# Optimization experiments

Measured on AMD Instinct MI355X. Metric: run time of the kernel, lower is better.

The kernel has to match this reference:

```python
import jax, jax.numpy as jnp
import numpy as np

D_HEAD = 64
SCALE = 1.0 / (D_HEAD ** 0.5)
B, H, S = 4, 16, 2048

def setup_inputs() -> dict:
    key = jax.random.key(0)
    kq, kk, kv, km = jax.random.split(key, 4)
    query = jax.random.normal(kq, (B, H, S, D_HEAD), dtype=jnp.float32)
    key_t = jax.random.normal(kk, (B, H, S, D_HEAD), dtype=jnp.float32)
    value = jax.random.normal(kv, (B, H, S, D_HEAD), dtype=jnp.float32)
    masked = jax.random.bernoulli(km, 0.5, (B, H, S, S))
    return {"query": query, "key": key_t, "value": value, "masked": masked}

def reference(query, key, value, masked):
    # scores = (Q K^T) * (1/sqrt(d_head)), mask filled with -1e9, softmax over last dim
    scores = jnp.einsum('bhqd,bhkd->bhqk', query, key) * SCALE
    scores = jnp.where(masked, jnp.float32(-1e9), scores)
    attn = jax.nn.softmax(scores, axis=-1)
    return jnp.einsum('bhqk,bhkd->bhqd', attn, value)
```

## Files before the change

### kernel.cpp

```cpp
#include <hip/hip_runtime.h>

namespace {

constexpr int D  = 64;
constexpr int S  = 2048;
constexpr int BQ = 64;
constexpr int BK = 64;
constexpr int NT = S / BK;
constexpr float SCALE = 0.125f;
constexpr int PP = 72;

typedef short s16x8 __attribute__((ext_vector_type(8)));
typedef float f32x4 __attribute__((ext_vector_type(4)));

__device__ inline unsigned cvt_pk_bf16(float a, float b) {
  unsigned r;
  asm("v_cvt_pk_bf16_f32 %0, %1, %2" : "=v"(r) : "v"(a), "v"(b));
  return r;
}

__device__ inline unsigned short f2bf(float f) {
  union { float f; unsigned u; } v; v.f = f;
  unsigned u = v.u + (0x7fffu + ((v.u >> 16) & 1u));
  return (unsigned short)(u >> 16);
}

__global__ __launch_bounds__(256)
void cvt_kv(const float* __restrict__ Kg, const float* __restrict__ Vg,
            unsigned short* __restrict__ Kw, unsigned short* __restrict__ Vw)
{
  __shared__ unsigned short vt[64 * 72];
  const int tid = threadIdx.x;
  const int kt = blockIdx.x, bh = blockIdx.y;
  const int k0 = kt * BK;

  #pragma unroll
  for (int i = 0; i < 4; ++i) {
    const int e4 = i * 256 + tid;
    const int r  = e4 >> 4;
    const int db = (e4 & 15) * 4;
    const size_t rowK = (size_t)bh * S + k0 + r;

    const float4 kf = *(const float4*)(Kg + rowK * D + db);
    const float4 vf = *(const float4*)(Vg + rowK * D + db);

    uint2 kk;
    kk.x = cvt_pk_bf16(kf.x, kf.y);
    kk.y = cvt_pk_bf16(kf.z, kf.w);
    *(uint2*)&Kw[rowK * D + db] = kk;

    const unsigned v01 = cvt_pk_bf16(vf.x, vf.y);
    const unsigned v23 = cvt_pk_bf16(vf.z, vf.w);
    vt[(db + 0) * 72 + r] = (unsigned short)(v01);
    vt[(db + 1) * 72 + r] = (unsigned short)(v01 >> 16);
    vt[(db + 2) * 72 + r] = (unsigned short)(v23);
    vt[(db + 3) * 72 + r] = (unsigned short)(v23 >> 16);
  }
  __syncthreads();

  const int d  = tid >> 2;
  const int bq = (tid & 3) * 16;
  const uint4 a = *(const uint4*)&vt[d * 72 + bq];
  const uint4 b = *(const uint4*)&vt[d * 72 + bq + 8];
  unsigned short* vrow = Vw + ((size_t)bh * D + d) * S + k0 + bq;
  *(uint4*)(vrow)     = a;
  *(uint4*)(vrow + 8) = b;
}

__global__ __launch_bounds__(256, 4)
void attn_fwd(const float* __restrict__ Qg,
              const unsigned short* __restrict__ Kw,
              const unsigned short* __restrict__ Vw,
              const int* __restrict__ Mg,
              float* __restrict__ Og)
{
  __shared__ unsigned short k_lds[BK * 64];
  __shared__ unsigned short vt_lds[D * 64];
  __shared__ unsigned short p_lds[4 * 16 * PP];

  const int tid  = threadIdx.x;
  const int lane = tid & 63;
  const int w    = tid >> 6;
  const int g    = lane >> 4;
  const int lq   = lane & 15;

  const int q0 = blockIdx.x * BQ;
  const int bh = blockIdx.y;

  const float* Qb = Qg + (size_t)bh * S * D;
  float* Ob = Og + (size_t)bh * S * D;
  const unsigned short* Kb = Kw + (size_t)bh * S * D;
  const unsigned short* Vb = Vw + (size_t)bh * D * S;
  const int* Mq = Mg + (size_t)bh * S * S + (size_t)(q0 + w * 16 + lq) * S;

  const int sr  = tid >> 2;
  const int sb  = (tid & 3) * 2;
  const int swz = sr & 7;
  const unsigned short* Ksrc0 = Kb + (size_t)sr * D + sb * 8;
  const unsigned short* Vsrc0 = Vb + (size_t)sr * S + sb * 8;

  s16x8 qf[2];
  {
    const float* qr = Qb + (size_t)(q0 + w * 16 + lq) * D;
    #pragma unroll
    for (int ks = 0; ks < 2; ++ks) {
      float4 a = *(const float4*)(qr + ks * 32 + g * 8);
      float4 b = *(const float4*)(qr + ks * 32 + g * 8 + 4);
      s16x8 t;
      t[0] = (short)f2bf(a.x * SCALE); t[1] = (short)f2bf(a.y * SCALE);
      t[2] = (short)f2bf(a.z * SCALE); t[3] = (short)f2bf(a.w * SCALE);
      t[4] = (short)f2bf(b.x * SCALE); t[5] = (short)f2bf(b.y * SCALE);
      t[6] = (short)f2bf(b.z * SCALE); t[7] = (short)f2bf(b.w * SCALE);
      qf[ks] = t;
    }
  }

  f32x4 o[4];
  #pragma unroll
  for (int i = 0; i < 4; ++i) { o[i][0]=0.f; o[i][1]=0.f; o[i][2]=0.f; o[i][3]=0.f; }
  float m_run = -INFINITY, l_run = 0.f;

  unsigned short* p_w = p_lds + w * 16 * PP;
  const int swzr = lq & 7;

  uint4 ka = *(const uint4*)(Ksrc0);
  uint4 kb = *(const uint4*)(Ksrc0 + 8);
  uint4 va = *(const uint4*)(Vsrc0);
  uint4 vb = *(const uint4*)(Vsrc0 + 8);
  uint4 mw[4];
  #pragma unroll
  for (int t = 0; t < 4; ++t) mw[t] = *(const uint4*)(Mq + 16 * t + 4 * g);

  for (int kt = 0; kt < NT; ++kt) {
    *(uint4*)&k_lds [sr * 64 + ((sb    ) ^ swz) * 8] = ka;
    *(uint4*)&k_lds [sr * 64 + ((sb + 1) ^ swz) * 8] = kb;
    *(uint4*)&vt_lds[sr * 64 + ((sb    ) ^ swz) * 8] = va;
    *(uint4*)&vt_lds[sr * 64 + ((sb + 1) ^ swz) * 8] = vb;

    asm volatile("s_waitcnt lgkmcnt(0)" ::: "memory");
    __builtin_amdgcn_sched_barrier(0);
    __builtin_amdgcn_s_barrier();

    const int kn = (kt + 1 < NT) ? (kt + 1) * BK : kt * BK;
    uint4 kan = *(const uint4*)(Ksrc0 + (size_t)kn * 64);
    uint4 kbn = *(const uint4*)(Ksrc0 + (size_t)kn * 64 + 8);
    uint4 van = *(const uint4*)(Vsrc0 + kn);
    uint4 vbn = *(const uint4*)(Vsrc0 + kn + 8);
    uint4 mwn[4];
    #pragma unroll
    for (int t = 0; t < 4; ++t) mwn[t] = *(const uint4*)(Mq + kn + 16 * t + 4 * g);

    f32x4 st[4];
    #pragma unroll
    for (int t = 0; t < 4; ++t) {
      f32x4 c; c[0]=0.f; c[1]=0.f; c[2]=0.f; c[3]=0.f;
      #pragma unroll
      for (int ks = 0; ks < 2; ++ks) {
        s16x8 a = *(const s16x8*)&k_lds[(16 * t + lq) * 64 + (((ks << 2) + g) ^ swzr) * 8];
        c = __builtin_amdgcn_mfma_f32_16x16x32_bf16(a, qf[ks], c, 0, 0, 0);
      }
      st[t] = c;
    }

    float mx = -INFINITY;
    #pragma unroll
    for (int t = 0; t < 4; ++t) {
      if (mw[t].x) st[t][0] = -1e9f;
      if (mw[t].y) st[t][1] = -1e9f;
      if (mw[t].z) st[t][2] = -1e9f;
      if (mw[t].w) st[t][3] = -1e9f;
      mx = fmaxf(mx, fmaxf(fmaxf(st[t][0], st[t][1]), fmaxf(st[t][2], st[t][3])));
    }
    mx = fmaxf(mx, __shfl_xor(mx, 16));
    mx = fmaxf(mx, __shfl_xor(mx, 32));
    const float m_new = fmaxf(m_run, mx);
    const float alpha = __expf(m_run - m_new);
    float rs = 0.f;
    #pragma unroll
    for (int t = 0; t < 4; ++t) {
      #pragma unroll
      for (int r = 0; r < 4; ++r) {
        float p = __expf(st[t][r] - m_new);
        st[t][r] = p;
        rs += p;
      }
    }
    rs += __shfl_xor(rs, 16);
    rs += __shfl_xor(rs, 32);
    l_run = l_run * alpha + rs;
    m_run = m_new;

    const float al0 = __shfl(alpha, 4 * g + 0);
    const float al1 = __shfl(alpha, 4 * g + 1);
    const float al2 = __shfl(alpha, 4 * g + 2);
    const float al3 = __shfl(alpha, 4 * g + 3);
    #pragma unroll
    for (int dt = 0; dt < 4; ++dt) {
      o[dt][0] *= al0; o[dt][1] *= al1; o[dt][2] *= al2; o[dt][3] *= al3;
    }

    #pragma unroll
    for (int t = 0; t < 4; ++t) {
      uint2 pk;
      pk.x = cvt_pk_bf16(st[t][0], st[t][1]);
      pk.y = cvt_pk_bf16(st[t][2], st[t][3]);
      *(uint2*)&p_w[lq * PP + 16 * t + 4 * g] = pk;
    }
    asm volatile("s_waitcnt lgkmcnt(0)" ::: "memory");
    __builtin_amdgcn_sched_barrier(0);

    const s16x8 pa0 = *(const s16x8*)&p_w[lq * PP + 0  + g * 8];
    const s16x8 pa1 = *(const s16x8*)&p_w[lq * PP + 32 + g * 8];
    #pragma unroll
    for (int dt = 0; dt < 4; ++dt) {
      s16x8 vb0 = *(const s16x8*)&vt_lds[(16 * dt + lq) * 64 + ((g    ) ^ swzr) * 8];
      s16x8 vb1 = *(const s16x8*)&vt_lds[(16 * dt + lq) * 64 + ((4 + g) ^ swzr) * 8];
      o[dt] = __builtin_amdgcn_mfma_f32_16x16x32_bf16(pa0, vb0, o[dt], 0, 0, 0);
      o[dt] = __builtin_amdgcn_mfma_f32_16x16x32_bf16(pa1, vb1, o[dt], 0, 0, 0);
    }

    __builtin_amdgcn_s_barrier();

    ka = kan; kb = kbn; va = van; vb = vbn;
    #pragma unroll
    for (int t = 0; t < 4; ++t) mw[t] = mwn[t];
  }

  const float linv = 1.0f / l_run;
  const float li0 = __shfl(linv, 4 * g + 0);
  const float li1 = __shfl(linv, 4 * g + 1);
  const float li2 = __shfl(linv, 4 * g + 2);
  const float li3 = __shfl(linv, 4 * g + 3);
  #pragma unroll
  for (int dt = 0; dt < 4; ++dt) {
    const int d = 16 * dt + lq;
    Ob[(size_t)(q0 + w * 16 + 4 * g + 0) * D + d] = o[dt][0] * li0;
    Ob[(size_t)(q0 + w * 16 + 4 * g + 1) * D + d] = o[dt][1] * li1;
    Ob[(size_t)(q0 + w * 16 + 4 * g + 2) * D + d] = o[dt][2] * li2;
    Ob[(size_t)(q0 + w * 16 + 4 * g + 3) * D + d] = o[dt][3] * li3;
  }
}

}

extern "C" void kernel_launch(void* const* d_in, const int* in_sizes, int n_in,
                              void* d_out, int out_size, void* d_ws, size_t ws_size,
                              hipStream_t stream) {
  const float* Q = (const float*)d_in[0];
  const float* K = (const float*)d_in[1];
  const float* V = (const float*)d_in[2];
  const int*   M = (const int*)d_in[3];
  float* O = (float*)d_out;

  unsigned short* Kw = (unsigned short*)d_ws;
  unsigned short* Vw = Kw + (size_t)4 * 16 * S * D;

  dim3 cgrid(NT, 4 * 16);
  hipLaunchKernelGGL(cvt_kv, cgrid, dim3(256), 0, stream, K, V, Kw, Vw);

  dim3 grid(S / BQ, 4 * 16);
  hipLaunchKernelGGL(attn_fwd, grid, dim3(256), 0, stream, Q, Kw, Vw, M, O);
}
```

Before: 286.2 us.

## Pack int32 attention mask into per-row bitmasks in a separate pre-pass kernel

Adds a mask_bits kernel that reads the int32 mask and packs each group of 64 key positions per query row into a 64-bit word stored in workspace. The attention kernel then loads one 64-bit word per key tile instead of four uint4 mask vectors, which cuts its global traffic and register use. The full int32 mask must still be read once, now in a separate launch, so total mask traffic is not reduced. That adds a launch, a bitmask write and a re-read, and removes the overlap of mask loads with the matmul work.

```diff
diff --git a/kernel.cpp b/kernel.cpp
--- a/kernel.cpp
+++ b/kernel.cpp
@@ -67,11 +67,37 @@
   *(uint4*)(vrow + 8) = b;
 }
 
+__global__ __launch_bounds__(256)
+void mask_bits(const int* __restrict__ Mg, unsigned long long* __restrict__ Mb)
+{
+  const int q    = blockIdx.x;
+  const int bh   = blockIdx.y;
+  const int lane = threadIdx.x & 63;
+  const int w    = threadIdx.x >> 6;
+  const int* Mrow = Mg + ((size_t)bh * S + q) * S;
+  unsigned long long* Mbrow = Mb + ((size_t)bh * S + q) * NT;
+
+  #pragma unroll
+  for (int i = 0; i < 2; ++i) {
+    const int base = (w + 4 * i) * 256;
+    const uint4 v = *(const uint4*)(Mrow + base + lane * 4);
+    unsigned long long word =
+        ((v.x ? 1ull : 0ull) | (v.y ? 2ull : 0ull) |
+         (v.z ? 4ull : 0ull) | (v.w ? 8ull : 0ull)) << (4 * (lane & 15));
+    word |= __shfl_xor(word, 1);
+    word |= __shfl_xor(word, 2);
+    word |= __shfl_xor(word, 4);
+    word |= __shfl_xor(word, 8);
+    if ((lane & 15) == 0)
+      Mbrow[(base >> 6) + (lane >> 4)] = word;
+  }
+}
+
 __global__ __launch_bounds__(256, 4)
 void attn_fwd(const float* __restrict__ Qg,
               const unsigned short* __restrict__ Kw,
               const unsigned short* __restrict__ Vw,
-              const int* __restrict__ Mg,
+              const unsigned long long* __restrict__ Mb,
               float* __restrict__ Og)
 {
   __shared__ unsigned short k_lds[BK * 64];
@@ -91,7 +117,7 @@
   float* Ob = Og + (size_t)bh * S * D;
   const unsigned short* Kb = Kw + (size_t)bh * S * D;
   const unsigned short* Vb = Vw + (size_t)bh * D * S;
-  const int* Mq = Mg + (size_t)bh * S * S + (size_t)(q0 + w * 16 + lq) * S;
+  const unsigned long long* Mrow = Mb + ((size_t)bh * S + (q0 + w * 16 + lq)) * NT;
 
   const int sr  = tid >> 2;
   const int sb  = (tid & 3) * 2;
@@ -127,9 +153,7 @@
   uint4 kb = *(const uint4*)(Ksrc0 + 8);
   uint4 va = *(const uint4*)(Vsrc0);
   uint4 vb = *(const uint4*)(Vsrc0 + 8);
-  uint4 mw[4];
-  #pragma unroll
-  for (int t = 0; t < 4; ++t) mw[t] = *(const uint4*)(Mq + 16 * t + 4 * g);
+  unsigned long long mw = Mrow[0];
 
   for (int kt = 0; kt < NT; ++kt) {
     *(uint4*)&k_lds [sr * 64 + ((sb    ) ^ swz) * 8] = ka;
@@ -146,9 +170,7 @@
     uint4 kbn = *(const uint4*)(Ksrc0 + (size_t)kn * 64 + 8);
     uint4 van = *(const uint4*)(Vsrc0 + kn);
     uint4 vbn = *(const uint4*)(Vsrc0 + kn + 8);
-    uint4 mwn[4];
-    #pragma unroll
-    for (int t = 0; t < 4; ++t) mwn[t] = *(const uint4*)(Mq + kn + 16 * t + 4 * g);
+    unsigned long long mwn = Mrow[kn >> 6];
 
     f32x4 st[4];
     #pragma unroll
@@ -162,13 +184,16 @@
       st[t] = c;
     }
 
+    const unsigned mlo = (unsigned)mw;
+    const unsigned mhi = (unsigned)(mw >> 32);
     float mx = -INFINITY;
     #pragma unroll
     for (int t = 0; t < 4; ++t) {
-      if (mw[t].x) st[t][0] = -1e9f;
-      if (mw[t].y) st[t][1] = -1e9f;
-      if (mw[t].z) st[t][2] = -1e9f;
-      if (mw[t].w) st[t][3] = -1e9f;
+      const unsigned nib = ((t < 2 ? mlo : mhi) >> (16 * (t & 1) + 4 * g)) & 0xFu;
+      if (nib & 1u) st[t][0] = -1e9f;
+      if (nib & 2u) st[t][1] = -1e9f;
+      if (nib & 4u) st[t][2] = -1e9f;
+      if (nib & 8u) st[t][3] = -1e9f;
       mx = fmaxf(mx, fmaxf(fmaxf(st[t][0], st[t][1]), fmaxf(st[t][2], st[t][3])));
     }
     mx = fmaxf(mx, __shfl_xor(mx, 16));
@@ -222,8 +247,7 @@
     __builtin_amdgcn_s_barrier();
 
     ka = kan; kb = kbn; va = van; vb = vbn;
-    #pragma unroll
-    for (int t = 0; t < 4; ++t) mw[t] = mwn[t];
+    mw = mwn;
   }
 
   const float linv = 1.0f / l_run;
@@ -254,10 +278,15 @@
 
   unsigned short* Kw = (unsigned short*)d_ws;
   unsigned short* Vw = Kw + (size_t)4 * 16 * S * D;
+  unsigned long long* Mb =
+      (unsigned long long*)(Vw + (size_t)4 * 16 * S * D);
 
   dim3 cgrid(NT, 4 * 16);
   hipLaunchKernelGGL(cvt_kv, cgrid, dim3(256), 0, stream, K, V, Kw, Vw);
 
+  dim3 mgrid(S, 4 * 16);
+  hipLaunchKernelGGL(mask_bits, mgrid, dim3(256), 0, stream, M, Mb);
+
   dim3 grid(S / BQ, 4 * 16);
-  hipLaunchKernelGGL(attn_fwd, grid, dim3(256), 0, stream, Q, Kw, Vw, M, O);
-}
+  hipLaunchKernelGGL(attn_fwd, grid, dim3(256), 0, stream, Q, Kw, Vw, Mb, O);
+}
```

Measured after the change: 357.5 us. 24.9% more time.
